# Kernel optimization log

Hardware: AMD Instinct MI355X
Metric: run time of the kernel (lower is better)

## Reference

```python
import jax, jax.numpy as jnp
import numpy as np

N_NODES = 100000
N_EDGES = 1600000
IN = 128
OUT = 32
HEADS = 4
NEG_SLOPE = 0.2


def setup_inputs() -> dict:
    key = jax.random.key(0)
    ks = jax.random.split(key, 6)
    x = jax.random.normal(ks[0], (N_NODES, IN), dtype=jnp.float32)
    row = jax.random.randint(ks[1], (N_EDGES,), 0, N_NODES, dtype=jnp.int32)
    col = jax.random.randint(ks[2], (N_EDGES,), 0, N_NODES, dtype=jnp.int32)
    W = jax.random.normal(ks[3], (OUT * HEADS, IN), dtype=jnp.float32) * (1.0 / np.sqrt(IN))
    b = jnp.zeros((OUT * HEADS,), dtype=jnp.float32)
    a_l = jax.random.normal(ks[4], (1, OUT, HEADS), dtype=jnp.float32) * 0.1
    a_r = jax.random.normal(ks[5], (1, OUT, HEADS), dtype=jnp.float32) * 0.1
    return {"x": x, "row": row, "col": col, "W": W, "b": b, "a_l": a_l, "a_r": a_r}


def reference(x, row, col, W, b, a_l, a_r):
    N = x.shape[0]
    # Z: [N, OUT, HEADS] (row-major view of [N, OUT*HEADS], matching torch .view)
    Z = (x @ W.T + b).reshape(N, OUT, HEADS)
    e_l = jnp.sum(Z * a_l, axis=1)  # [N, HEADS]
    e_r = jnp.sum(Z * a_r, axis=1)  # [N, HEADS]
    e = e_l[row] + e_r[col]         # [E, HEADS]
    e = jnp.where(e > 0, e, NEG_SLOPE * e)  # LeakyReLU
    # segment softmax over edges grouped by destination (row)
    m = jax.ops.segment_max(e, row, num_segments=N)      # [N, HEADS]
    ex = jnp.exp(e - m[row])                              # [E, HEADS]
    denom = jax.ops.segment_sum(ex, row, num_segments=N)  # [N, HEADS]
    alpha = ex / denom[row]                               # [E, HEADS]
    # bspmm: out[i,:,h] = sum_{(i,j) in E} alpha[e,h] * Z[j,:,h]
    out = jax.ops.segment_sum(alpha[:, None, :] * Z[col], row, num_segments=N)
    return out
```

## Files before the change

### kernel.cpp

```cpp
#include <hip/hip_runtime.h>
#include <hip/hip_bf16.h>
#include <math.h>


typedef __attribute__((ext_vector_type(8))) short bf16x8;
typedef __attribute__((ext_vector_type(4))) float f32x4;

__device__ __forceinline__ ushort f2bf(float f) {
  __hip_bfloat16 h = __float2bfloat16(f);
  return __builtin_bit_cast(ushort, h);
}
__device__ __forceinline__ float bf2f(ushort u) {
  unsigned v = ((unsigned)u) << 16;
  return __builtin_bit_cast(float, v);
}

__global__ __launch_bounds__(512, 4) void gemm_deg(
    const float* __restrict__ x, const float* __restrict__ W,
    const float* __restrict__ bias,
    const float* __restrict__ a_l, const float* __restrict__ a_r,
    ushort* __restrict__ Zh, float* __restrict__ el, float* __restrict__ er,
    int N, const int* __restrict__ row, int* __restrict__ cntP,
    int* __restrict__ rank, int E, int G1, int ilv) {
  __shared__ __align__(16) ushort smem[16896];
  __shared__ float sal[128], sar[128];

  const int b = (int)blockIdx.x;
  int tile = -1, tailt = -1;
  if (ilv) {
    if ((b % 5 == 0) && (b / 5 < G1)) tile = b / 5;
    else {
      int g = (b + 4) / 5;
      if (g > G1) g = G1;
      tailt = b - g;
    }
  } else {
    if (b < G1) tile = b; else tailt = b - G1;
  }

  if (tile < 0) {
    int e = tailt * 512 + (int)threadIdx.x;
    if (e < E) {
      int copy = b & 7;
      rank[e] = atomicAdd(&cntP[copy * N + row[e]], 1);
    }
    return;
  }

  const int t = threadIdx.x;
  const int lane = t & 63;
  const int wv = t >> 6;
  const int row0 = tile * 128;
  const int l15 = lane & 15, l4 = lane >> 4;
  const int ch = wv * 16 + l15;

  if (t < 128) { sal[t] = a_l[t]; sar[t] = a_r[t]; }

  bf16x8 Bh[4], Bl[4];
#pragma unroll
  for (int kf = 0; kf < 4; ++kf) {
    const float* wp = W + (size_t)ch * 128 + kf * 32 + l4 * 8;
    float4 w0 = *(const float4*)(wp);
    float4 w1 = *(const float4*)(wp + 4);
    float wf[8] = {w0.x, w0.y, w0.z, w0.w, w1.x, w1.y, w1.z, w1.w};
    bf16x8 hi, lo;
#pragma unroll
    for (int j = 0; j < 8; ++j) {
      ushort hb = f2bf(wf[j]);
      hi[j] = (short)hb;
      lo[j] = (short)f2bf(wf[j] - bf2f(hb));
    }
    Bh[kf] = hi;
    Bl[kf] = lo;
  }

  ushort* xh = smem;
#pragma unroll
  for (int i = 0; i < 8; ++i) {
    int f4 = i * 512 + t;
    int r = f4 >> 5;
    int k = (f4 & 31) * 4;
    int gr = row0 + r;
    float4 v = make_float4(0.f, 0.f, 0.f, 0.f);
    if (gr < N) v = ((const float4*)x)[(size_t)gr * 32 + (f4 & 31)];
    int idx = r * 128 + (k ^ ((r & 7) << 3));
    uint2 hv;
    hv.x = f2bf(v.x) | ((unsigned)f2bf(v.y) << 16);
    hv.y = f2bf(v.z) | ((unsigned)f2bf(v.w) << 16);
    *(uint2*)&xh[idx] = hv;
  }
  __syncthreads();

  f32x4 acc[8];
#pragma unroll
  for (int rt = 0; rt < 8; ++rt) acc[rt] = (f32x4){0.f, 0.f, 0.f, 0.f};

#pragma unroll
  for (int kf = 0; kf < 4; ++kf) {
#pragma unroll
    for (int rt = 0; rt < 8; ++rt) {
      int r = rt * 16 + l15;
      int idx = r * 128 + ((kf * 32 + l4 * 8) ^ ((r & 7) << 3));
      bf16x8 ah = *(const bf16x8*)&xh[idx];
      acc[rt] = __builtin_amdgcn_mfma_f32_16x16x32_bf16(ah, Bh[kf], acc[rt], 0, 0, 0);
      acc[rt] = __builtin_amdgcn_mfma_f32_16x16x32_bf16(ah, Bl[kf], acc[rt], 0, 0, 0);
    }
  }
  __syncthreads();

  ushort* zs = smem;
  {
    float bv = bias[ch];
    int o = ch >> 2, h = ch & 3;
    int s = (o & 15) * 8 + h * 2 + (o >> 4);
#pragma unroll
    for (int rt = 0; rt < 8; ++rt) {
#pragma unroll
      for (int j = 0; j < 4; ++j) {
        int r = rt * 16 + l4 * 4 + j;
        zs[r * 132 + s] = f2bf(acc[rt][j] + bv);
      }
    }
  }
  __syncthreads();

  {
    int r = t >> 2;
    int h = t & 3;
    int gr = row0 + r;
    if (gr < N) {
#pragma unroll
      for (int q = 0; q < 4; ++q) {
        uint4 v = *(const uint4*)&zs[r * 132 + h * 32 + q * 8];
        *(uint4*)&Zh[(size_t)gr * 128 + h * 32 + q * 8] = v;
      }
      float sl = 0.f, sr = 0.f;
#pragma unroll
      for (int op = 0; op < 16; ++op) {
        unsigned zz = *(const unsigned*)&zs[r * 132 + op * 8 + h * 2];
        float zlo = bf2f((ushort)(zz & 0xffff));
        float zhi = bf2f((ushort)(zz >> 16));
        int c = (op << 2) + h;
        sl += zlo * sal[c] + zhi * sal[c + 64];
        sr += zlo * sar[c] + zhi * sar[c + 64];
      }
      el[(unsigned)gr * 4 + h] = sl;
      er[(unsigned)gr * 4 + h] = sr;
    }
  }
}

__global__ __launch_bounds__(256) void nscan(
    int* __restrict__ cntP, int* __restrict__ deg, int* __restrict__ base,
    int* __restrict__ bsum, int N) {
  __shared__ int ss[256];
  int t = threadIdx.x;
  int i = blockIdx.x * 256 + t;
  int tot = 0;
  if (i < N) {
    int run = 0;
#pragma unroll
    for (int k = 0; k < 8; ++k) {
      int c = cntP[k * N + i];
      cntP[k * N + i] = run;
      run += c;
    }
    tot = run;
  }
  ss[t] = tot;
  __syncthreads();
#pragma unroll
  for (int off = 1; off < 256; off <<= 1) {
    int u = (t >= off) ? ss[t - off] : 0;
    __syncthreads();
    ss[t] += u;
    __syncthreads();
  }
  if (i < N) {
    base[i] = ss[t] - tot;
    deg[i] = tot;
  }
  if (t == 255) bsum[blockIdx.x] = ss[255];
}

__global__ __launch_bounds__(512) void scan2(int* __restrict__ bsum, int NB) {
  __shared__ int s[512];
  int v = (threadIdx.x < NB) ? bsum[threadIdx.x] : 0;
  s[threadIdx.x] = v;
  __syncthreads();
#pragma unroll
  for (int off = 1; off < 512; off <<= 1) {
    int t = (threadIdx.x >= off) ? s[threadIdx.x - off] : 0;
    __syncthreads();
    s[threadIdx.x] += t;
    __syncthreads();
  }
  if (threadIdx.x < NB) bsum[threadIdx.x] = s[threadIdx.x] - v;
}

__global__ __launch_bounds__(256) void fill(
    const int* __restrict__ row, const int* __restrict__ col,
    const int* __restrict__ rank, const int* __restrict__ base,
    const int* __restrict__ bsum, const int* __restrict__ cntP,
    int* __restrict__ sorted_col, int E, int N, int G1, int ilv) {
  int e = blockIdx.x * 256 + threadIdx.x;
  if (e >= E) return;
  int r = row[e];
  int t9 = e >> 9;
  int b = ilv ? ((t9 >> 2) * 5 + (t9 & 3) + 1)
              : (G1 + t9);
  int copy = b & 7;
  int pos = base[r] + bsum[r >> 8] + cntP[copy * N + r] + rank[e];
  sorted_col[pos] = col[e];
}

__global__ __launch_bounds__(256) void gather(
    const int* __restrict__ base, const int* __restrict__ bsum,
    const int* __restrict__ deg, const int* __restrict__ sorted_col,
    const float* __restrict__ el, const float* __restrict__ er,
    const ushort* __restrict__ Zh, float* __restrict__ out, int N) {
  int t = threadIdx.x;
  int lane = t & 63;
  int n = blockIdx.x * 4 + (t >> 6);
  if (n >= N) return;
  int h = lane & 3;
  int jj = lane >> 2;
  int s = base[n] + bsum[n >> 8];
  int d = deg[n];
  int end = s + d;
  float elv = el[((unsigned)n << 2) + h];
  float acc0 = 0.f, acc1 = 0.f, sumA = 0.f;
  const unsigned* Zh32 = (const unsigned*)Zh;
  const unsigned zlane = (unsigned)lane;
  const int bpb = (lane & 3) << 2;

  auto phaseA = [&](int pp) -> unsigned {
    unsigned pkv = 0;
    if (pp + jj < end) {
      int cl = sorted_col[pp + jj];
      float e = elv + er[((unsigned)cl << 2) + h];
      e = fmaxf(e, 0.2f * e);
      float x = __expf(e);
      sumA += x;
      pkv = ((unsigned)cl << 15) | (f2bf(x) & 0x7fffu);
    }
    return pkv;
  };

  unsigned pk = (s < end) ? phaseA(s) : 0;
  for (int p = s; p < end; p += 16) {
    float xvb[16];
    unsigned addrv[16];
#pragma unroll
    for (int q = 0; q < 16; ++q) {
      int a = bpb + (q << 4);
      unsigned bb = (unsigned)__builtin_amdgcn_ds_bpermute(a, (int)pk);
      addrv[q] = ((bb >> 15) << 6) + zlane;
      xvb[q] = bf2f((ushort)(bb & 0x7fffu));
    }
    unsigned zz[16];
#pragma unroll
    for (int q = 0; q < 16; ++q) zz[q] = Zh32[addrv[q]];
    int np = p + 16;
    unsigned pk2 = (np < end) ? phaseA(np) : 0;
#pragma unroll
    for (int q = 0; q < 16; ++q) {
      acc0 = fmaf(xvb[q], __builtin_bit_cast(float, zz[q] << 16), acc0);
      acc1 = fmaf(xvb[q], __builtin_bit_cast(float, zz[q] & 0xffff0000u), acc1);
    }
    pk = pk2;
  }
  float sum = sumA;
  sum += __shfl_xor(sum, 4, 64);
  sum += __shfl_xor(sum, 8, 64);
  sum += __shfl_xor(sum, 16, 64);
  sum += __shfl_xor(sum, 32, 64);
  float inv = (d > 0) ? 1.0f / sum : 0.f;
  unsigned ob = ((unsigned)n << 7) + zlane;
  __builtin_nontemporal_store(acc0 * inv, &out[ob]);
  __builtin_nontemporal_store(acc1 * inv, &out[ob + 64]);
}

extern "C" void kernel_launch(void* const* d_in, const int* in_sizes, int n_in,
                              void* d_out, int out_size, void* d_ws, size_t ws_size,
                              hipStream_t stream) {
  const float* x   = (const float*)d_in[0];
  const int*   row = (const int*)d_in[1];
  const int*   col = (const int*)d_in[2];
  const float* W   = (const float*)d_in[3];
  const float* b   = (const float*)d_in[4];
  const float* a_l = (const float*)d_in[5];
  const float* a_r = (const float*)d_in[6];
  float* out = (float*)d_out;

  const int N = in_sizes[0] / 128;
  const int E = in_sizes[1];
  const int NB = (N + 255) / 256;

  char* w = (char*)d_ws;
  ushort* Zh       = (ushort*)w;             w += (size_t)N * 128 * 2;
  int*   sorted_col= (int*)w;                w += (size_t)E * 4;
  int*   rank      = (int*)w;                w += (size_t)E * 4;
  float* el        = (float*)w;              w += (size_t)N * 4 * 4;
  float* er        = (float*)w;              w += (size_t)N * 4 * 4;
  int*   cntP      = (int*)w;                w += (size_t)N * 8 * 4;
  int*   deg       = (int*)w;                w += (size_t)N * 4;
  int*   base      = (int*)w;                w += (size_t)N * 4;
  int*   bsum      = (int*)w;                w += 512 * 4;

  hipMemsetAsync(cntP, 0, (size_t)N * 8 * sizeof(int), stream);

  const int G1 = (N + 127) / 128;
  const int G2 = (E + 511) / 512;
  const int ilv = ((G1 - 1) * 5 < G1 + G2) ? 1 : 0;
  gemm_deg<<<G1 + G2, 512, 0, stream>>>(x, W, b, a_l, a_r, Zh, el, er,
                                        N, row, cntP, rank, E, G1, ilv);

  nscan<<<NB, 256, 0, stream>>>(cntP, deg, base, bsum, N);
  scan2<<<1, 512, 0, stream>>>(bsum, NB);
  fill<<<(E + 255) / 256, 256, 0, stream>>>(row, col, rank, base, bsum, cntP,
                                            sorted_col, E, N, G1, ilv);
  gather<<<(N + 3) / 4, 256, 0, stream>>>(base, bsum, deg, sorted_col, el, er,
                                          Zh, out, N);
}
```

Baseline: 200.2 us.

## Pad per-copy degree counters, shrink rank to bytes, batch 4 edges per block

Spaces the 8 per-copy atomic counters 32 bytes apart per node so concurrent atomics fall in distinct sectors. Stores the per-edge rank as one byte instead of an int to cut rank write and read traffic. Each counting block now handles 2048 edges, and counting blocks alternate 1:1 with GEMM tiles instead of a 4:1 pattern. The padded counter array is eight times larger, which adds memset and scan traffic with strided access, and a byte rank silently overflows if a node receives more than 255 edges within one copy.

```diff
diff --git a/kernel.cpp b/kernel.cpp
--- a/kernel.cpp
+++ b/kernel.cpp
@@ -14,6 +14,8 @@
   unsigned v = ((unsigned)u) << 16;
   return __builtin_bit_cast(float, v);
 }
+
+#define CNT_IDX(copy, n, N) ((size_t)(copy) * ((size_t)(N) * 8) + (size_t)(n) * 8)
 
 __global__ __launch_bounds__(512, 4) void gemm_deg(
     const float* __restrict__ x, const float* __restrict__ W,
@@ -21,28 +23,30 @@
     const float* __restrict__ a_l, const float* __restrict__ a_r,
     ushort* __restrict__ Zh, float* __restrict__ el, float* __restrict__ er,
     int N, const int* __restrict__ row, int* __restrict__ cntP,
-    int* __restrict__ rank, int E, int G1, int ilv) {
+    unsigned char* __restrict__ rank, int E, int G1, int G2) {
   __shared__ __align__(16) ushort smem[16896];
   __shared__ float sal[128], sar[128];
 
   const int b = (int)blockIdx.x;
+  const int minG = (G1 < G2) ? G1 : G2;
   int tile = -1, tailt = -1;
-  if (ilv) {
-    if ((b % 5 == 0) && (b / 5 < G1)) tile = b / 5;
-    else {
-      int g = (b + 4) / 5;
-      if (g > G1) g = G1;
-      tailt = b - g;
-    }
+  if (b < 2 * minG) {
+    if ((b & 1) == 0) tile = b >> 1; else tailt = b >> 1;
   } else {
-    if (b < G1) tile = b; else tailt = b - G1;
+    if (G1 > G2) tile = b - minG; else tailt = b - minG;
   }
 
   if (tile < 0) {
-    int e = tailt * 512 + (int)threadIdx.x;
-    if (e < E) {
-      int copy = b & 7;
-      rank[e] = atomicAdd(&cntP[copy * N + row[e]], 1);
+    int ebase = tailt * 2048;
+    int copy = b & 7;
+    int* cbase = cntP + CNT_IDX(copy, 0, N);
+#pragma unroll
+    for (int q = 0; q < 4; ++q) {
+      int e = ebase + q * 512 + (int)threadIdx.x;
+      if (e < E) {
+        int pos = atomicAdd(&cbase[(size_t)row[e] * 8], 1);
+        rank[e] = (unsigned char)pos;
+      }
     }
     return;
   }
@@ -161,8 +165,9 @@
     int run = 0;
 #pragma unroll
     for (int k = 0; k < 8; ++k) {
-      int c = cntP[k * N + i];
-      cntP[k * N + i] = run;
+      size_t ix = CNT_IDX(k, i, N);
+      int c = cntP[ix];
+      cntP[ix] = run;
       run += c;
     }
     tot = run;
@@ -200,17 +205,17 @@
 
 __global__ __launch_bounds__(256) void fill(
     const int* __restrict__ row, const int* __restrict__ col,
-    const int* __restrict__ rank, const int* __restrict__ base,
+    const unsigned char* __restrict__ rank, const int* __restrict__ base,
     const int* __restrict__ bsum, const int* __restrict__ cntP,
-    int* __restrict__ sorted_col, int E, int N, int G1, int ilv) {
+    int* __restrict__ sorted_col, int E, int N, int G1, int G2) {
   int e = blockIdx.x * 256 + threadIdx.x;
   if (e >= E) return;
   int r = row[e];
-  int t9 = e >> 9;
-  int b = ilv ? ((t9 >> 2) * 5 + (t9 & 3) + 1)
-              : (G1 + t9);
+  int minG = (G1 < G2) ? G1 : G2;
+  int t11 = e >> 11;
+  int b = (t11 < minG) ? (2 * t11 + 1) : (minG + t11);
   int copy = b & 7;
-  int pos = base[r] + bsum[r >> 8] + cntP[copy * N + r] + rank[e];
+  int pos = base[r] + bsum[r >> 8] + cntP[CNT_IDX(copy, r, N)] + (int)rank[e];
   sorted_col[pos] = col[e];
 }
 
@@ -300,26 +305,26 @@
   char* w = (char*)d_ws;
   ushort* Zh       = (ushort*)w;             w += (size_t)N * 128 * 2;
   int*   sorted_col= (int*)w;                w += (size_t)E * 4;
-  int*   rank      = (int*)w;                w += (size_t)E * 4;
+  unsigned char* rank = (unsigned char*)w;   w += (size_t)E;
+  w = (char*)(((size_t)w + 15) & ~(size_t)15);
   float* el        = (float*)w;              w += (size_t)N * 4 * 4;
   float* er        = (float*)w;              w += (size_t)N * 4 * 4;
-  int*   cntP      = (int*)w;                w += (size_t)N * 8 * 4;
+  int*   cntP      = (int*)w;                w += (size_t)N * 8 * 8 * 4;
   int*   deg       = (int*)w;                w += (size_t)N * 4;
   int*   base      = (int*)w;                w += (size_t)N * 4;
   int*   bsum      = (int*)w;                w += 512 * 4;
 
-  hipMemsetAsync(cntP, 0, (size_t)N * 8 * sizeof(int), stream);
+  hipMemsetAsync(cntP, 0, (size_t)N * 8 * 8 * sizeof(int), stream);
 
   const int G1 = (N + 127) / 128;
-  const int G2 = (E + 511) / 512;
-  const int ilv = ((G1 - 1) * 5 < G1 + G2) ? 1 : 0;
+  const int G2 = (E + 2047) / 2048;
   gemm_deg<<<G1 + G2, 512, 0, stream>>>(x, W, b, a_l, a_r, Zh, el, er,
-                                        N, row, cntP, rank, E, G1, ilv);
+                                        N, row, cntP, rank, E, G1, G2);
 
   nscan<<<NB, 256, 0, stream>>>(cntP, deg, base, bsum, N);
   scan2<<<1, 512, 0, stream>>>(bsum, NB);
   fill<<<(E + 255) / 256, 256, 0, stream>>>(row, col, rank, base, bsum, cntP,
-                                            sorted_col, E, N, G1, ilv);
+                                            sorted_col, E, N, G1, G2);
   gather<<<(N + 3) / 4, 256, 0, stream>>>(base, bsum, deg, sorted_col, el, er,
                                           Zh, out, N);
 }
```

Result: slower. 213.9 us (+6.9%).
